# Performance work log

Hardware: AMD Instinct MI355X
Metric: run time of the kernel (lower is better)

Reference implementation:

```python
import jax, jax.numpy as jnp
import numpy as np

T, D, E, K = 16384, 2048, 64, 2
LOAD_BALANCE_SCALE = 0.01
NOISY_STD = 1.0


def setup_inputs() -> dict:
    key = jax.random.key(0)
    k1, k2, k3, k4 = jax.random.split(key, 4)
    x_flat = jax.random.normal(k1, (T, D), dtype=jnp.float32)
    noise = jax.random.normal(k2, (T, E), dtype=jnp.float32)
    # gate_linear: nn.Linear(D, E, bias=False) -> weight [E, D]
    W_gate = jax.random.normal(k3, (E, D), dtype=jnp.float32) * (1.0 / np.sqrt(D))
    # noise_weight initialized to zeros in torch; use small values so the
    # noisy path is exercised numerically.
    noise_weight = jax.random.normal(k4, (E,), dtype=jnp.float32) * 0.01
    return {"x_flat": x_flat, "noise": noise, "W_gate": W_gate,
            "noise_weight": noise_weight, "k": K}


def reference(x_flat, noise, W_gate, noise_weight, k):
    # logits = x @ W^T   [T, E]
    logits = jnp.einsum("td,ed->te", x_flat, W_gate)
    logits_noisy = logits + (noise * NOISY_STD) * noise_weight

    # noisy top-k; softmax over -inf-sparse logits == softmax over the k
    # selected logits scattered into zeros (top-k ids are unique per row).
    top_vals, top_ids = jax.lax.top_k(logits_noisy, k)          # [T, k]
    gates_k = jax.nn.softmax(top_vals, axis=-1)                 # [T, k]
    rows = jnp.arange(x_flat.shape[0])[:, None]
    top_k_gated_weights = jnp.zeros_like(logits_noisy).at[rows, top_ids].set(gates_k)

    # load-balance loss on clean logits
    gate_weights_mean = jax.nn.softmax(logits, axis=-1).mean(axis=0)  # [E]
    uniform = jnp.full_like(gate_weights_mean, 1.0 / gate_weights_mean.shape[0])
    load_balance_loss = jnp.mean((gate_weights_mean - uniform) ** 2) * LOAD_BALANCE_SCALE

    return top_k_gated_weights, top_ids, load_balance_loss
```

## Files before the change

### kernel.cpp

```cpp
#include <hip/hip_runtime.h>
#include <hip/hip_bf16.h>

#define T_TOK 16384
#define D_DIM 2048
#define E_EXP 64
#define TAU   2e-3f

typedef __bf16 bf16x8 __attribute__((ext_vector_type(8)));
typedef float  f32x16 __attribute__((ext_vector_type(16)));
typedef unsigned short ushort_t;

#define WS_WHI  0
#define WS_WLO  (256*1024)
#define WS_SUM  (512*1024)
#define WS_CNT  (512*1024 + 512)
#define WS_FLG  (512*1024 + 1024)

__device__ __forceinline__ unsigned short bf16_rne(float x){
  unsigned int u = __float_as_uint(x);
  return (unsigned short)((u + 0x7FFFu + ((u >> 16) & 1u)) >> 16);
}

__device__ __forceinline__ void ins3(float& v1, int& i1, float& v2, int& i2,
                                     float& v3, int& i3, float v, int i){
  if (v > v1 || (v == v1 && i < i1)) { v3=v2; i3=i2; v2=v1; i2=i1; v1=v; i1=i; }
  else if (v > v2 || (v == v2 && i < i2)) { v3=v2; i3=i2; v2=v; i2=i; }
  else if (v > v3 || (v == v3 && i < i3)) { v3=v; i3=i; }
}

__device__ __forceinline__ void gload16(const void* g, const void* l){
  __builtin_amdgcn_global_load_lds(
      (const __attribute__((address_space(1))) unsigned int*)g,
      (__attribute__((address_space(3))) unsigned int*)l, 16, 0, 0);
}

__global__ void wsplit_kernel(const float* __restrict__ W,
                              ushort_t* __restrict__ whi, ushort_t* __restrict__ wlo,
                              double* __restrict__ ESUM, int* __restrict__ FCNT){
  const int n = blockIdx.x * 256 + threadIdx.x;
  if (blockIdx.x == 0){
    if (threadIdx.x < 64) ESUM[threadIdx.x] = 0.0;
    else if (threadIdx.x == 64) *FCNT = 0;
  }
  const int lane = n & 63;
  const int eh   = (n >> 6) & 1;
  const int w    = (n >> 7) & 7;
  const int c    = n >> 10;
  const float* src = W + (size_t)(eh*32 + (lane & 31))*D_DIM
                       + c*128 + w*16 + (lane >> 5)*8;
  float4 w0 = *reinterpret_cast<const float4*>(src);
  float4 w1 = *reinterpret_cast<const float4*>(src + 4);
  float f[8] = {w0.x,w0.y,w0.z,w0.w,w1.x,w1.y,w1.z,w1.w};
  unsigned h[8], lo[8];
  #pragma unroll
  for (int i = 0; i < 8; ++i){
    h[i]  = bf16_rne(f[i]);
    lo[i] = bf16_rne(f[i] - __uint_as_float(h[i] << 16));
  }
  uint4 hv = { h[0]|(h[1]<<16),  h[2]|(h[3]<<16),  h[4]|(h[5]<<16),  h[6]|(h[7]<<16) };
  uint4 lv = { lo[0]|(lo[1]<<16), lo[2]|(lo[3]<<16), lo[4]|(lo[5]<<16), lo[6]|(lo[7]<<16) };
  *reinterpret_cast<uint4*>(whi + (size_t)n*8) = hv;
  *reinterpret_cast<uint4*>(wlo + (size_t)n*8) = lv;
}

__launch_bounds__(512, 4)
__global__ void moe_main(const float* __restrict__ X, const float* __restrict__ NZ,
                         const ushort_t* __restrict__ WHI, const ushort_t* __restrict__ WLO,
                         const float* __restrict__ NW, float* __restrict__ OUT,
                         double* __restrict__ ESUM, int* __restrict__ FCNT,
                         int* __restrict__ FLIST)
{
  __shared__ __align__(16) char smem[32768];

  const int tid  = threadIdx.x;
  const int lane = tid & 63;
  const int wv   = tid >> 6;
  const int eh   = wv & 1;
  const int ks   = wv >> 1;
  const int r0   = blockIdx.x << 5;
  const int m    = lane & 31;
  const int kg   = lane >> 5;

  const int n0   = wv*64 + lane;
  const int row0 = n0 >> 5, g0 = n0 & 31;
  const int gs0  = (g0 & 24) | ((g0 ^ row0) & 7);
  const char* px0 = (const char*)X + ((size_t)(r0 + row0)*D_DIM + gs0*4) * 4;
  const char* px1 = px0 + (size_t)16*D_DIM*4;
  const char* ldsx0 = smem +        wv*1024;
  const char* ldsx1 = smem + 8192 + wv*1024;

  const char* pwh = (const char*)WHI + (size_t)(ks*256 + eh*64 + lane)*16;
  const char* pwl = (const char*)WLO + (size_t)(ks*256 + eh*64 + lane)*16;

  const int gf0 = ks*8 + kg*2;
  const int gf1 = gf0 + 4;
  const int offA0 = m*512 + (((gf0  ) & 24) | (((gf0  ) ^ m) & 7))*16;
  const int offB0 = m*512 + (((gf0+1) & 24) | (((gf0+1) ^ m) & 7))*16;
  const int offA1 = m*512 + (((gf1  ) & 24) | (((gf1  ) ^ m) & 7))*16;
  const int offB1 = m*512 + (((gf1+1) & 24) | (((gf1+1) ^ m) & 7))*16;

  f32x16 acc;
  #pragma unroll
  for (int i = 0; i < 16; ++i) acc[i] = 0.0f;

  uint4 whA0, wlA0, whA1, wlA1;
  uint4 whB0, wlB0, whB1, wlB1;

  #define LOADW(c, H0, L0, H1, L1) do{                                         \
    H0 = *reinterpret_cast<const uint4*>(pwh + (size_t)(c)*16384);             \
    L0 = *reinterpret_cast<const uint4*>(pwl + (size_t)(c)*16384);             \
    H1 = *reinterpret_cast<const uint4*>(pwh + (size_t)(c)*16384 + 2048);      \
    L1 = *reinterpret_cast<const uint4*>(pwl + (size_t)(c)*16384 + 2048);      \
  }while(0)

  #define ISSUE(c, BUF, H0, L0, H1, L1) do{                                    \
    __builtin_amdgcn_sched_barrier(0);                                         \
    gload16(px0 + (size_t)(c)*512, ldsx0 + (BUF));                             \
    gload16(px1 + (size_t)(c)*512, ldsx1 + (BUF));                             \
    LOADW(c, H0, L0, H1, L1);                                                  \
    __builtin_amdgcn_sched_barrier(0);                                         \
  }while(0)

  #define CVT8(fa, fb, ah, al) do{                                             \
    float fv[8] = {fa.x,fa.y,fa.z,fa.w,fb.x,fb.y,fb.z,fb.w};                   \
    _Pragma("unroll")                                                          \
    for (int ii = 0; ii < 8; ++ii){                                            \
      __bf16 hh = (__bf16)fv[ii];                                              \
      ah[ii] = hh; al[ii] = (__bf16)(fv[ii] - (float)hh);                      \
    }                                                                          \
  }while(0)

  #define KS2(BUF, OA, OB, WH, WL) do{                                         \
    float4 fa = *reinterpret_cast<const float4*>(smem + (BUF) + (OA));         \
    float4 fb = *reinterpret_cast<const float4*>(smem + (BUF) + (OB));         \
    bf16x8 ah, al;                                                             \
    CVT8(fa, fb, ah, al);                                                      \
    bf16x8 bh = __builtin_bit_cast(bf16x8, WH);                                \
    bf16x8 bl = __builtin_bit_cast(bf16x8, WL);                                \
    acc = __builtin_amdgcn_mfma_f32_32x32x16_bf16(ah, bh, acc, 0, 0, 0);       \
    acc = __builtin_amdgcn_mfma_f32_32x32x16_bf16(ah, bl, acc, 0, 0, 0);       \
    acc = __builtin_amdgcn_mfma_f32_32x32x16_bf16(al, bh, acc, 0, 0, 0);       \
  }while(0)

  #define PHASE(cc, H0, L0, H1, L1, BUF, WNTOK, DOISS) do{                     \
    asm volatile("s_waitcnt vmcnt(" WNTOK ")" ::: "memory");                   \
    __builtin_amdgcn_sched_barrier(0);                                         \
    __builtin_amdgcn_s_barrier();                                              \
    KS2(BUF, offA0, offB0, H0, L0);                                            \
    KS2(BUF, offA1, offB1, H1, L1);                                            \
    __builtin_amdgcn_s_barrier();                                              \
    if (DOISS) ISSUE((cc) + 2, BUF, H0, L0, H1, L1);                           \
  }while(0)

  ISSUE(0, 0,     whA0, wlA0, whA1, wlA1);
  ISSUE(1, 16384, whB0, wlB0, whB1, wlB1);

  #pragma unroll 1
  for (int g = 0; g < 7; ++g){
    PHASE(2*g,     whA0, wlA0, whA1, wlA1, 0,     "6", 1);
    PHASE(2*g + 1, whB0, wlB0, whB1, wlB1, 16384, "6", 1);
  }
  PHASE(14, whA0, wlA0, whA1, wlA1, 0,     "6", 0);
  PHASE(15, whB0, wlB0, whB1, wlB1, 16384, "0", 0);

  #undef PHASE
  #undef KS2
  #undef CVT8
  #undef ISSUE
  #undef LOADW

  float* lgts = (float*)(smem);
  float* nzs  = (float*)(smem + 8192);
  float* prb  = (float*)(smem + 16384);
  float* nws  = (float*)(smem + 24576);
  const int ex = eh*32 + m;

  __syncthreads();
  if (ks == 0){
    #pragma unroll
    for (int r = 0; r < 16; ++r){
      int rr = (r & 3) + ((r >> 2) << 3) + (kg << 2);
      lgts[rr*64 + ex] = acc[r];
    }
  }
  __syncthreads();
  #pragma unroll
  for (int p = 1; p < 4; ++p){
    if (ks == p){
      #pragma unroll
      for (int r = 0; r < 16; ++r){
        int rr = (r & 3) + ((r >> 2) << 3) + (kg << 2);
        lgts[rr*64 + ex] += acc[r];
      }
    }
    __syncthreads();
  }

  const int sr = tid >> 4, sc = tid & 15;
  *reinterpret_cast<float4*>(&nzs[sr*64 + sc*4]) =
    *reinterpret_cast<const float4*>(NZ + (size_t)(r0 + sr)*E_EXP + sc*4);
  if (tid < 64) nws[tid] = NW[tid];
  __syncthreads();

  if (wv < 4){
    const int rrow = (wv << 3) + (lane >> 3);
    const int j    = lane & 7;
    const int trow = r0 + rrow;
    float cl[8];
    float v1 = -INFINITY, v2 = -INFINITY, v3 = -INFINITY;
    int   i1 = 1 << 29,   i2 = 1 << 29,   i3 = 1 << 29;
    #pragma unroll
    for (int mm = 0; mm < 8; ++mm){
      int q = j + (mm << 3);
      float lg = lgts[rrow*64 + q];
      cl[mm] = lg;
      float vn = fmaf(nzs[rrow*64 + q], nws[q], lg);
      ins3(v1,i1,v2,i2,v3,i3, vn, q);
    }
    #pragma unroll
    for (int d = 1; d < 8; d <<= 1){
      float ov1 = __shfl_xor(v1, d, 8), ov2 = __shfl_xor(v2, d, 8), ov3 = __shfl_xor(v3, d, 8);
      int   oi1 = __shfl_xor(i1, d, 8), oi2 = __shfl_xor(i2, d, 8), oi3 = __shfl_xor(i3, d, 8);
      ins3(v1,i1,v2,i2,v3,i3, ov1, oi1);
      ins3(v1,i1,v2,i2,v3,i3, ov2, oi2);
      ins3(v1,i1,v2,i2,v3,i3, ov3, oi3);
    }
    float e1 = expf(v2 - v1);
    float g0g = 1.0f / (1.0f + e1);
    float g1g = e1 * g0g;

    float mx = cl[0];
    #pragma unroll
    for (int mm = 1; mm < 8; ++mm) mx = fmaxf(mx, cl[mm]);
    #pragma unroll
    for (int d = 1; d < 8; d <<= 1) mx = fmaxf(mx, __shfl_xor(mx, d, 8));
    float sum = 0.0f, exv[8];
    #pragma unroll
    for (int mm = 0; mm < 8; ++mm){ exv[mm] = expf(cl[mm] - mx); sum += exv[mm]; }
    #pragma unroll
    for (int d = 1; d < 8; d <<= 1) sum += __shfl_xor(sum, d, 8);
    float inv = 1.0f / sum;
    #pragma unroll
    for (int mm = 0; mm < 8; ++mm) prb[rrow*64 + j + (mm << 3)] = exv[mm] * inv;

    if (j == 0){
      OUT[(size_t)T_TOK*E_EXP + (size_t)trow*2]     = (float)i1;
      OUT[(size_t)T_TOK*E_EXP + (size_t)trow*2 + 1] = (float)i2;
      if ((v1 - v2 < TAU) || (v2 - v3 < TAU)){
        int slot = atomicAdd(FCNT, 1);
        FLIST[slot] = trow;
      }
    }
    #pragma unroll
    for (int mm = 0; mm < 8; ++mm){
      int q = j + (mm << 3);
      lgts[rrow*64 + q] = (q == i1) ? g0g : ((q == i2) ? g1g : 0.0f);
    }
  }
  __syncthreads();

  *reinterpret_cast<float4*>(OUT + (size_t)(r0 + sr)*E_EXP + sc*4) =
    *reinterpret_cast<const float4*>(&lgts[sr*64 + sc*4]);
  if (tid < 64){
    float s0 = 0.0f;
    #pragma unroll 8
    for (int rr2 = 0; rr2 < 32; ++rr2) s0 += prb[rr2*64 + tid];
    atomicAdd(&ESUM[tid], (double)s0);
  }
}

__launch_bounds__(256)
__global__ void moe_finalize(const float* __restrict__ X, const float* __restrict__ NZ,
                             const float* __restrict__ WG, const float* __restrict__ NW,
                             float* __restrict__ OUT, const double* __restrict__ ESUM,
                             const int* __restrict__ FCNT, const int* __restrict__ FLIST)
{
  if (blockIdx.x == 0){
    if (threadIdx.x < 64){
      const int e = threadIdx.x;
      double d = ESUM[e] * (1.0 / T_TOK) - (1.0 / 64.0);
      double sq = d * d;
      #pragma unroll
      for (int off = 1; off < 64; off <<= 1) sq += __shfl_xor(sq, off, 64);
      if (e == 0) OUT[(size_t)T_TOK*E_EXP + T_TOK*2] = (float)(sq * (0.01 / 64.0));
    }
    return;
  }

  __shared__ __align__(16) float xl[2048];
  __shared__ double lz[64];
  __shared__ int   si1, si2;
  __shared__ float sg0, sg1;
  const int n    = *FCNT;
  const int lane = threadIdx.x & 63;
  const int wv   = threadIdx.x >> 6;
  for (int idx = blockIdx.x - 1; idx < n; idx += 511){
    const int t = FLIST[idx];
    {
      int off = threadIdx.x * 8;
      *reinterpret_cast<float4*>(xl + off) =
        *reinterpret_cast<const float4*>(X + (size_t)t*D_DIM + off);
      *reinterpret_cast<float4*>(xl + off + 4) =
        *reinterpret_cast<const float4*>(X + (size_t)t*D_DIM + off + 4);
    }
    __syncthreads();
    for (int s = 0; s < 16; ++s){
      const int e = wv*16 + s;
      const float* wr = WG + (size_t)e*D_DIM;
      double acc = 0.0;
      #pragma unroll
      for (int it = 0; it < 8; ++it){
        float4 w4 = *reinterpret_cast<const float4*>(wr + it*256 + lane*4);
        float4 x4 = *reinterpret_cast<const float4*>(xl + it*256 + lane*4);
        acc += (double)x4.x * (double)w4.x;
        acc += (double)x4.y * (double)w4.y;
        acc += (double)x4.z * (double)w4.z;
        acc += (double)x4.w * (double)w4.w;
      }
      #pragma unroll
      for (int off = 1; off < 64; off <<= 1) acc += __shfl_xor(acc, off, 64);
      if (lane == 0)
        lz[e] = acc + (double)NZ[(size_t)t*E_EXP + e] * (double)NW[e];
    }
    __syncthreads();
    if (threadIdx.x == 0){
      double b1 = -1e300, b2 = -1e300; int j1 = 0, j2 = 0;
      for (int q = 0; q < 64; ++q){
        double v = lz[q];
        if (v > b1){ b2 = b1; j2 = j1; b1 = v; j1 = q; }
        else if (v > b2){ b2 = v; j2 = q; }
      }
      double ee = exp(b2 - b1);
      sg0 = (float)(1.0 / (1.0 + ee));
      sg1 = (float)(ee / (1.0 + ee));
      si1 = j1; si2 = j2;
      OUT[(size_t)T_TOK*E_EXP + (size_t)t*2]     = (float)j1;
      OUT[(size_t)T_TOK*E_EXP + (size_t)t*2 + 1] = (float)j2;
    }
    __syncthreads();
    if (threadIdx.x < 64)
      OUT[(size_t)t*E_EXP + threadIdx.x] = (threadIdx.x == si1) ? sg0 :
                                           ((threadIdx.x == si2) ? sg1 : 0.0f);
    __syncthreads();
  }
}

extern "C" void kernel_launch(void* const* d_in, const int* in_sizes, int n_in,
                              void* d_out, int out_size, void* d_ws, size_t ws_size,
                              hipStream_t stream)
{
  const float* X  = (const float*)d_in[0];
  const float* NZ = (const float*)d_in[1];
  const float* WG = (const float*)d_in[2];
  const float* NW = (const float*)d_in[3];
  float* OUT = (float*)d_out;
  char*  ws  = (char*)d_ws;
  ushort_t* WHI = (ushort_t*)(ws + WS_WHI);
  ushort_t* WLO = (ushort_t*)(ws + WS_WLO);
  double* ESUM = (double*)(ws + WS_SUM);
  int* FCNT  = (int*)(ws + WS_CNT);
  int* FLIST = (int*)(ws + WS_FLG);

  wsplit_kernel<<<dim3(64), dim3(256), 0, stream>>>(WG, WHI, WLO, ESUM, FCNT);
  moe_main<<<dim3(T_TOK/32), dim3(512), 0, stream>>>(X, NZ, WHI, WLO, NW, OUT, ESUM, FCNT, FLIST);
  moe_finalize<<<dim3(512), dim3(256), 0, stream>>>(X, NZ, WG, NW, OUT, ESUM, FCNT, FLIST);
}
```

Baseline: 111.7 us.

## Retile gate GEMM to 8-row blocks with 16x16x32 MFMA and full-row LDS staging

Restructures the main kernel so that each block handles 8 tokens instead of 32. Each block loads its whole 8xD slice of X into padded LDS up front, then runs a 16-step loop of 16x16x32 bf16 MFMAs using the split hi/lo precision scheme. The weight-split kernel writes W in a new layout matching the 16x16 fragment order, and blocks are launched in a swizzled order. This gives four times as many blocks and drops the double-buffered pipeline. The costs are that each block rereads the full split W from cache, half of each MFMA's rows are duplicated padding, and the global loads no longer overlap with compute.

```diff
diff --git a/kernel.cpp b/kernel.cpp
--- a/kernel.cpp
+++ b/kernel.cpp
@@ -7,7 +7,7 @@
 #define TAU   2e-3f
 
 typedef __bf16 bf16x8 __attribute__((ext_vector_type(8)));
-typedef float  f32x16 __attribute__((ext_vector_type(16)));
+typedef float  f32x4  __attribute__((ext_vector_type(4)));
 typedef unsigned short ushort_t;
 
 #define WS_WHI  0
@@ -15,6 +15,8 @@
 #define WS_SUM  (512*1024)
 #define WS_CNT  (512*1024 + 512)
 #define WS_FLG  (512*1024 + 1024)
+
+#define XSTRIDE_DW 2052
 
 __device__ __forceinline__ unsigned short bf16_rne(float x){
   unsigned int u = __float_as_uint(x);
@@ -42,12 +44,9 @@
     if (threadIdx.x < 64) ESUM[threadIdx.x] = 0.0;
     else if (threadIdx.x == 64) *FCNT = 0;
   }
-  const int lane = n & 63;
-  const int eh   = (n >> 6) & 1;
-  const int w    = (n >> 7) & 7;
-  const int c    = n >> 10;
-  const float* src = W + (size_t)(eh*32 + (lane & 31))*D_DIM
-                       + c*128 + w*16 + (lane >> 5)*8;
+  const int e  = n >> 8;
+  const int k0 = (n & 255) * 8;
+  const float* src = W + (size_t)e*D_DIM + k0;
   float4 w0 = *reinterpret_cast<const float4*>(src);
   float4 w1 = *reinterpret_cast<const float4*>(src + 4);
   float f[8] = {w0.x,w0.y,w0.z,w0.w,w1.x,w1.y,w1.z,w1.w};
@@ -59,8 +58,11 @@
   }
   uint4 hv = { h[0]|(h[1]<<16),  h[2]|(h[3]<<16),  h[4]|(h[5]<<16),  h[6]|(h[7]<<16) };
   uint4 lv = { lo[0]|(lo[1]<<16), lo[2]|(lo[3]<<16), lo[4]|(lo[5]<<16), lo[6]|(lo[7]<<16) };
-  *reinterpret_cast<uint4*>(whi + (size_t)n*8) = hv;
-  *reinterpret_cast<uint4*>(wlo + (size_t)n*8) = lv;
+  const int ks = k0 >> 9, t = (k0 >> 5) & 15, kg = (k0 >> 3) & 3;
+  const int eh = e >> 5,  et = (e >> 4) & 1;
+  const int G  = ((ks*16 + t)*4 + eh*2 + et)*64 + kg*16 + (e & 15);
+  *reinterpret_cast<uint4*>(whi + (size_t)G*8) = hv;
+  *reinterpret_cast<uint4*>(wlo + (size_t)G*8) = lv;
 }
 
 __launch_bounds__(512, 4)
@@ -70,140 +72,91 @@
                          double* __restrict__ ESUM, int* __restrict__ FCNT,
                          int* __restrict__ FLIST)
 {
-  __shared__ __align__(16) char smem[32768];
+  __shared__ __align__(16) char smem[8 * XSTRIDE_DW * 4];
 
   const int tid  = threadIdx.x;
   const int lane = tid & 63;
   const int wv   = tid >> 6;
   const int eh   = wv & 1;
   const int ks   = wv >> 1;
-  const int r0   = blockIdx.x << 5;
-  const int m    = lane & 31;
-  const int kg   = lane >> 5;
-
-  const int n0   = wv*64 + lane;
-  const int row0 = n0 >> 5, g0 = n0 & 31;
-  const int gs0  = (g0 & 24) | ((g0 ^ row0) & 7);
-  const char* px0 = (const char*)X + ((size_t)(r0 + row0)*D_DIM + gs0*4) * 4;
-  const char* px1 = px0 + (size_t)16*D_DIM*4;
-  const char* ldsx0 = smem +        wv*1024;
-  const char* ldsx1 = smem + 8192 + wv*1024;
-
-  const char* pwh = (const char*)WHI + (size_t)(ks*256 + eh*64 + lane)*16;
-  const char* pwl = (const char*)WLO + (size_t)(ks*256 + eh*64 + lane)*16;
-
-  const int gf0 = ks*8 + kg*2;
-  const int gf1 = gf0 + 4;
-  const int offA0 = m*512 + (((gf0  ) & 24) | (((gf0  ) ^ m) & 7))*16;
-  const int offB0 = m*512 + (((gf0+1) & 24) | (((gf0+1) ^ m) & 7))*16;
-  const int offA1 = m*512 + (((gf1  ) & 24) | (((gf1  ) ^ m) & 7))*16;
-  const int offB1 = m*512 + (((gf1+1) & 24) | (((gf1+1) ^ m) & 7))*16;
-
-  f32x16 acc;
+  const int bid2 = (blockIdx.x & 7) * 256 + (blockIdx.x >> 3);
+  const int r0   = bid2 << 3;
+
+  {
+    const char* psrc = (const char*)X + (size_t)(r0 + wv)*D_DIM*4 + lane*16;
+    #pragma unroll
+    for (int q = 0; q < 8; ++q)
+      gload16(psrc + q*1024, smem + wv*(XSTRIDE_DW*4) + q*1024);
+  }
+  asm volatile("s_waitcnt vmcnt(0)" ::: "memory");
+  __syncthreads();
+
+  const int arow = lane & 7;
+  const int akg  = lane >> 4;
+  const char* pa  = smem + (arow*XSTRIDE_DW + ks*512 + akg*8)*4;
+  const char* pwh = (const char*)WHI + ((size_t)(ks*64 + eh*2))*1024 + lane*16;
+  const char* pwl = (const char*)WLO + ((size_t)(ks*64 + eh*2))*1024 + lane*16;
+
+  f32x4 acc0 = {0.f,0.f,0.f,0.f}, acc1 = {0.f,0.f,0.f,0.f};
+
   #pragma unroll
-  for (int i = 0; i < 16; ++i) acc[i] = 0.0f;
-
-  uint4 whA0, wlA0, whA1, wlA1;
-  uint4 whB0, wlB0, whB1, wlB1;
-
-  #define LOADW(c, H0, L0, H1, L1) do{                                         \
-    H0 = *reinterpret_cast<const uint4*>(pwh + (size_t)(c)*16384);             \
-    L0 = *reinterpret_cast<const uint4*>(pwl + (size_t)(c)*16384);             \
-    H1 = *reinterpret_cast<const uint4*>(pwh + (size_t)(c)*16384 + 2048);      \
-    L1 = *reinterpret_cast<const uint4*>(pwl + (size_t)(c)*16384 + 2048);      \
-  }while(0)
-
-  #define ISSUE(c, BUF, H0, L0, H1, L1) do{                                    \
-    __builtin_amdgcn_sched_barrier(0);                                         \
-    gload16(px0 + (size_t)(c)*512, ldsx0 + (BUF));                             \
-    gload16(px1 + (size_t)(c)*512, ldsx1 + (BUF));                             \
-    LOADW(c, H0, L0, H1, L1);                                                  \
-    __builtin_amdgcn_sched_barrier(0);                                         \
-  }while(0)
-
-  #define CVT8(fa, fb, ah, al) do{                                             \
-    float fv[8] = {fa.x,fa.y,fa.z,fa.w,fb.x,fb.y,fb.z,fb.w};                   \
-    _Pragma("unroll")                                                          \
-    for (int ii = 0; ii < 8; ++ii){                                            \
-      __bf16 hh = (__bf16)fv[ii];                                              \
-      ah[ii] = hh; al[ii] = (__bf16)(fv[ii] - (float)hh);                      \
-    }                                                                          \
-  }while(0)
-
-  #define KS2(BUF, OA, OB, WH, WL) do{                                         \
-    float4 fa = *reinterpret_cast<const float4*>(smem + (BUF) + (OA));         \
-    float4 fb = *reinterpret_cast<const float4*>(smem + (BUF) + (OB));         \
-    bf16x8 ah, al;                                                             \
-    CVT8(fa, fb, ah, al);                                                      \
-    bf16x8 bh = __builtin_bit_cast(bf16x8, WH);                                \
-    bf16x8 bl = __builtin_bit_cast(bf16x8, WL);                                \
-    acc = __builtin_amdgcn_mfma_f32_32x32x16_bf16(ah, bh, acc, 0, 0, 0);       \
-    acc = __builtin_amdgcn_mfma_f32_32x32x16_bf16(ah, bl, acc, 0, 0, 0);       \
-    acc = __builtin_amdgcn_mfma_f32_32x32x16_bf16(al, bh, acc, 0, 0, 0);       \
-  }while(0)
-
-  #define PHASE(cc, H0, L0, H1, L1, BUF, WNTOK, DOISS) do{                     \
-    asm volatile("s_waitcnt vmcnt(" WNTOK ")" ::: "memory");                   \
-    __builtin_amdgcn_sched_barrier(0);                                         \
-    __builtin_amdgcn_s_barrier();                                              \
-    KS2(BUF, offA0, offB0, H0, L0);                                            \
-    KS2(BUF, offA1, offB1, H1, L1);                                            \
-    __builtin_amdgcn_s_barrier();                                              \
-    if (DOISS) ISSUE((cc) + 2, BUF, H0, L0, H1, L1);                           \
-  }while(0)
-
-  ISSUE(0, 0,     whA0, wlA0, whA1, wlA1);
-  ISSUE(1, 16384, whB0, wlB0, whB1, wlB1);
-
-  #pragma unroll 1
-  for (int g = 0; g < 7; ++g){
-    PHASE(2*g,     whA0, wlA0, whA1, wlA1, 0,     "6", 1);
-    PHASE(2*g + 1, whB0, wlB0, whB1, wlB1, 16384, "6", 1);
-  }
-  PHASE(14, whA0, wlA0, whA1, wlA1, 0,     "6", 0);
-  PHASE(15, whB0, wlB0, whB1, wlB1, 16384, "0", 0);
-
-  #undef PHASE
-  #undef KS2
-  #undef CVT8
-  #undef ISSUE
-  #undef LOADW
+  for (int t = 0; t < 16; ++t){
+    float4 fa = *reinterpret_cast<const float4*>(pa + t*128);
+    float4 fb = *reinterpret_cast<const float4*>(pa + t*128 + 16);
+    bf16x8 ah, al;
+    {
+      float fv[8] = {fa.x,fa.y,fa.z,fa.w,fb.x,fb.y,fb.z,fb.w};
+      #pragma unroll
+      for (int ii = 0; ii < 8; ++ii){
+        __bf16 hh = (__bf16)fv[ii];
+        ah[ii] = hh; al[ii] = (__bf16)(fv[ii] - (float)hh);
+      }
+    }
+    uint4 h0 = *reinterpret_cast<const uint4*>(pwh + (size_t)t*4096);
+    uint4 l0 = *reinterpret_cast<const uint4*>(pwl + (size_t)t*4096);
+    uint4 h1 = *reinterpret_cast<const uint4*>(pwh + (size_t)t*4096 + 1024);
+    uint4 l1 = *reinterpret_cast<const uint4*>(pwl + (size_t)t*4096 + 1024);
+    bf16x8 bh0 = __builtin_bit_cast(bf16x8, h0), bl0 = __builtin_bit_cast(bf16x8, l0);
+    bf16x8 bh1 = __builtin_bit_cast(bf16x8, h1), bl1 = __builtin_bit_cast(bf16x8, l1);
+    acc0 = __builtin_amdgcn_mfma_f32_16x16x32_bf16(ah, bh0, acc0, 0, 0, 0);
+    acc0 = __builtin_amdgcn_mfma_f32_16x16x32_bf16(al, bh0, acc0, 0, 0, 0);
+    acc0 = __builtin_amdgcn_mfma_f32_16x16x32_bf16(ah, bl0, acc0, 0, 0, 0);
+    acc1 = __builtin_amdgcn_mfma_f32_16x16x32_bf16(ah, bh1, acc1, 0, 0, 0);
+    acc1 = __builtin_amdgcn_mfma_f32_16x16x32_bf16(al, bh1, acc1, 0, 0, 0);
+    acc1 = __builtin_amdgcn_mfma_f32_16x16x32_bf16(ah, bl1, acc1, 0, 0, 0);
+  }
 
   float* lgts = (float*)(smem);
-  float* nzs  = (float*)(smem + 8192);
-  float* prb  = (float*)(smem + 16384);
-  float* nws  = (float*)(smem + 24576);
-  const int ex = eh*32 + m;
-
-  __syncthreads();
-  if (ks == 0){
-    #pragma unroll
-    for (int r = 0; r < 16; ++r){
-      int rr = (r & 3) + ((r >> 2) << 3) + (kg << 2);
-      lgts[rr*64 + ex] = acc[r];
-    }
-  }
+  float* nzs  = (float*)(smem + 2048);
+  float* prb  = (float*)(smem + 4096);
+  float* nws  = (float*)(smem + 6144);
+
   __syncthreads();
   #pragma unroll
-  for (int p = 1; p < 4; ++p){
-    if (ks == p){
-      #pragma unroll
-      for (int r = 0; r < 16; ++r){
-        int rr = (r & 3) + ((r >> 2) << 3) + (kg << 2);
-        lgts[rr*64 + ex] += acc[r];
-      }
-    }
-    __syncthreads();
-  }
-
-  const int sr = tid >> 4, sc = tid & 15;
-  *reinterpret_cast<float4*>(&nzs[sr*64 + sc*4]) =
-    *reinterpret_cast<const float4*>(NZ + (size_t)(r0 + sr)*E_EXP + sc*4);
+  for (int p = 0; p < 4; ++p){
+    if (ks == p && lane < 32){
+      const int crow = (lane >> 4)*4;
+      const int col0 = eh*32 + (lane & 15);
+      #pragma unroll
+      for (int r = 0; r < 4; ++r){
+        if (p == 0){
+          lgts[(crow + r)*64 + col0]      = acc0[r];
+          lgts[(crow + r)*64 + col0 + 16] = acc1[r];
+        } else {
+          lgts[(crow + r)*64 + col0]      += acc0[r];
+          lgts[(crow + r)*64 + col0 + 16] += acc1[r];
+        }
+      }
+    }
+    __syncthreads();
+  }
+
+  nzs[tid] = NZ[(size_t)(r0 + (tid >> 6))*E_EXP + (tid & 63)];
   if (tid < 64) nws[tid] = NW[tid];
   __syncthreads();
 
-  if (wv < 4){
-    const int rrow = (wv << 3) + (lane >> 3);
+  if (wv == 0){
+    const int rrow = lane >> 3;
     const int j    = lane & 7;
     const int trow = r0 + rrow;
     float cl[8];
@@ -259,12 +212,11 @@
   }
   __syncthreads();
 
-  *reinterpret_cast<float4*>(OUT + (size_t)(r0 + sr)*E_EXP + sc*4) =
-    *reinterpret_cast<const float4*>(&lgts[sr*64 + sc*4]);
+  OUT[(size_t)(r0 + (tid >> 6))*E_EXP + (tid & 63)] = lgts[tid];
   if (tid < 64){
     float s0 = 0.0f;
-    #pragma unroll 8
-    for (int rr2 = 0; rr2 < 32; ++rr2) s0 += prb[rr2*64 + tid];
+    #pragma unroll
+    for (int rr2 = 0; rr2 < 8; ++rr2) s0 += prb[rr2*64 + tid];
     atomicAdd(&ESUM[tid], (double)s0);
   }
 }
@@ -362,6 +314,6 @@
   int* FLIST = (int*)(ws + WS_FLG);
 
   wsplit_kernel<<<dim3(64), dim3(256), 0, stream>>>(WG, WHI, WLO, ESUM, FCNT);
-  moe_main<<<dim3(T_TOK/32), dim3(512), 0, stream>>>(X, NZ, WHI, WLO, NW, OUT, ESUM, FCNT, FLIST);
+  moe_main<<<dim3(T_TOK/8), dim3(512), 0, stream>>>(X, NZ, WHI, WLO, NW, OUT, ESUM, FCNT, FLIST);
   moe_finalize<<<dim3(512), dim3(256), 0, stream>>>(X, NZ, WG, NW, OUT, ESUM, FCNT, FLIST);
 }
```

Result: slower. 194.3 us (+73.9%).
